# Optimization experiments

Hardware: AMD Instinct MI355X
Metric: run time of the kernel (lower is better)

The kernel has to match this reference:

```python
import jax, jax.numpy as jnp
import numpy as np

N = 2048      # feature_num (nodes/sensors)
T = 5         # timd_num (window length)
D = 64        # embed_dim
TOPK = 21     # topk + 1 (includes self, cos(i,i)=1)
B = 32        # batch
EPS = 1e-5
NEG_SLOPE = 0.2


def setup_inputs() -> dict:
    key = jax.random.key(0)
    ks = jax.random.split(key, 9)
    s = 1.0 / np.sqrt(D)
    return {
        "x": jax.random.normal(ks[0], (B, N, T), jnp.float32),
        "emb": jax.random.normal(ks[1], (N, D), jnp.float32) * s,      # embedding table
        "W": jax.random.normal(ks[2], (D, T), jnp.float32) * (1.0 / np.sqrt(T)),  # GNN lin weight
        "Wb": jax.random.normal(ks[3], (D,), jnp.float32) * 0.01,       # GNN lin bias
        "a_src": jax.random.normal(ks[4], (2 * D,), jnp.float32) * s,   # attention vec (source half)
        "a_dst": jax.random.normal(ks[5], (2 * D,), jnp.float32) * s,   # attention vec (dest half)
        "gamma": jnp.ones((D,), jnp.float32),                            # BatchNorm1d weight
        "beta": jnp.zeros((D,), jnp.float32),                            # BatchNorm1d bias
        "fc_w": jax.random.normal(ks[6], (1, D), jnp.float32) * s,      # fc weight
        "fc_b": jnp.zeros((1,), jnp.float32),                            # fc bias
    }


def reference(x, emb, W, Wb, a_src, a_dst, gamma, beta, fc_w, fc_b):
    # --- cosine-sim topk graph build ---
    norm = jnp.linalg.norm(emb, axis=-1)                    # [N]
    cos = (emb @ emb.T) / (norm[:, None] * norm[None, :])   # [N,N]
    _, idx = jax.lax.top_k(cos, TOPK)                       # [N,TOPK]
    # scatter one-hot adjacency (vectorized, no per-row loop)
    adj = jnp.zeros((N, N), x.dtype).at[jnp.arange(N)[:, None], idx].set(1.0)
    # --- GNN: GDN-style attention message passing ---
    h = jnp.einsum('bnt,dt->bnd', x, W) + Wb                # [B,N,D]
    g = jnp.concatenate([h, jnp.broadcast_to(emb, h.shape)], axis=-1)  # [B,N,2D]
    e_src = g @ a_src                                       # [B,N]
    e_dst = g @ a_dst                                       # [B,N]
    e = jax.nn.leaky_relu(e_src[:, :, None] + e_dst[:, None, :], NEG_SLOPE)  # [B,N,N]
    e = jnp.where(adj > 0, e, jnp.float32(-1e9))
    alpha = jax.nn.softmax(e, axis=-1)                      # [B,N,N], rows sum to 1 over TOPK nbrs
    z = jax.nn.relu(jnp.einsum('bij,bjd->bid', alpha, h))   # [B,N,D]
    # --- output head: z * emb, BN over channels, relu, fc ---
    out = z * emb                                           # [B,N,D]
    mean = out.mean(axis=(0, 1))                            # BN1d stats over (batch, nodes)
    var = out.var(axis=(0, 1))
    out = (out - mean) * jax.lax.rsqrt(var + EPS) * gamma + beta
    out = jax.nn.relu(out)
    out = out @ fc_w.T + fc_b                               # [B,N,1]
    return out.reshape(-1, N)                               # [B,N]
```

## Files before the change

### kernel.cpp

```cpp
#include <hip/hip_runtime.h>
#include <hip/hip_fp16.h>
#include <math.h>

#define N_NODES 2048
#define T_WIN 5
#define D_EMB 64
#define TOPK 21
#define B_BATCH 32
#define BN_TOTAL (B_BATCH * N_NODES)
#define EPS_BN 1e-5f
#define NEG_SLOPE 0.2f
#define STATS_STRIDE 16

typedef unsigned long long u64;
typedef unsigned short u16;
typedef unsigned int u32;

__device__ __forceinline__ float wave_sum(float v) {
#pragma unroll
    for (int off = 32; off > 0; off >>= 1) v += __shfl_xor(v, off, 64);
    return v;
}

__device__ __forceinline__ u64 max64(u64 a, u64 b) { return a > b ? a : b; }
__device__ __forceinline__ u64 min64(u64 a, u64 b) { return a < b ? a : b; }

__device__ __forceinline__ u64 bitonic_sort64_desc(u64 key, int lane) {
#pragma unroll
    for (int k = 2; k <= 64; k <<= 1) {
#pragma unroll
        for (int j = k >> 1; j >= 1; j >>= 1) {
            u64 pk = __shfl_xor(key, j, 64);
            bool dirDesc = ((lane & k) == 0);
            bool keepMax = (((lane & j) == 0) == dirDesc);
            key = keepMax ? max64(key, pk) : min64(key, pk);
        }
    }
    return key;
}

__device__ __forceinline__ u64 bitonic_merge_top64(u64 a, u64 b, int lane) {
    u64 br = __shfl(b, 63 - lane, 64);
    u64 c = max64(a, br);
#pragma unroll
    for (int j = 32; j >= 1; j >>= 1) {
        u64 pk = __shfl_xor(c, j, 64);
        bool keepMax = ((lane & j) == 0);
        c = keepMax ? max64(c, pk) : min64(c, pk);
    }
    return c;
}

__device__ __forceinline__ u16 f2bf(float f) {
    unsigned u = __float_as_uint(f);
    return (u16)((u + 0x7FFFu + ((u >> 16) & 1u)) >> 16);
}
__device__ __forceinline__ float bf2f(u16 h) {
    return __uint_as_float((unsigned)h << 16);
}

__global__ __launch_bounds__(256) void k_preg(
    const float* __restrict__ x, const float* __restrict__ W,
    const float* __restrict__ Wb, const float* __restrict__ a_src,
    const float* __restrict__ a_dst, const float* __restrict__ emb,
    float* __restrict__ xs2T, float* __restrict__ xd2T,
    float* __restrict__ es_embP, float* __restrict__ ed_embP,
    float* __restrict__ norms, float* __restrict__ dotM,
    float* __restrict__ stats, float* __restrict__ stats2) {
    __shared__ __align__(16) float As[64][68];
    __shared__ __align__(16) float Bs[64][68];
    int t = threadIdx.x;

    if (blockIdx.x >= 528) {
        int eb = blockIdx.x - 528;
        if (eb < 512) {
            if (eb < 2) {
                float* p = eb ? stats2 : stats;
                ((float4*)p)[t] = make_float4(0.f, 0.f, 0.f, 0.f);
            }
            int wid = t >> 6, lane = t & 63;
            int node = eb * 4 + wid;
            float e = emb[node * D_EMB + lane];
            float s2 = wave_sum(e * e);
            float esE = wave_sum(e * a_src[D_EMB + lane]);
            float edE = wave_sum(e * a_dst[D_EMB + lane]);
            if (lane == 0) {
                norms[node] = sqrtf(s2);
                es_embP[node] = esE;
                ed_embP[node] = edE;
            }
        } else {
            __shared__ float cws[5], cwd[5], cbs[2];
            if (t < 12) {
                int which = (t < 5 || t == 10) ? 0 : 1;
                const float* av = which ? a_dst : a_src;
                const float* sp;
                int stride;
                if (t < 10) { int tt = (t < 5) ? t : t - 5; sp = W + tt; stride = T_WIN; }
                else        { sp = Wb; stride = 1; }
                float acc = 0.f;
                for (int d = 0; d < D_EMB; d++) acc += sp[d * stride] * av[d];
                if (t < 5)       cws[t] = acc;
                else if (t < 10) cwd[t - 5] = acc;
                else             cbs[t - 10] = acc;
            }
            __syncthreads();
            float ws0 = cws[0], ws1 = cws[1], ws2 = cws[2], ws3 = cws[3], ws4 = cws[4];
            float wd0 = cwd[0], wd1 = cwd[1], wd2 = cwd[2], wd3 = cwd[3], wd4 = cwd[4];
            float bss = cbs[0], bsd = cbs[1];
            int base = (eb - 512) * 1024;
#pragma unroll
            for (int r = 0; r < 4; r++) {
                int item = base + 256 * r + t;
                const float* xp = x + (size_t)item * T_WIN;
                float x0 = xp[0], x1 = xp[1], x2 = xp[2], x3 = xp[3], x4 = xp[4];
                xs2T[item] = bss + x0 * ws0 + x1 * ws1 + x2 * ws2 + x3 * ws3 + x4 * ws4;
                xd2T[item] = bsd + x0 * wd0 + x1 * wd1 + x2 * wd2 + x3 * wd3 + x4 * wd4;
            }
        }
        return;
    }

    int g = blockIdx.x;
    int a = (int)((sqrtf(8.f * g + 1.f) - 1.f) * 0.5f);
    while ((a + 1) * (a + 2) / 2 <= g) a++;
    while (a * (a + 1) / 2 > g) a--;
    int bq = g - a * (a + 1) / 2;
    int i0 = a * 64, j0 = bq * 64;

    {
        int r = t >> 2, c0 = t & 3;
        const float4* srcA = (const float4*)(emb + (size_t)(i0 + r) * D_EMB);
        const float4* srcB = (const float4*)(emb + (size_t)(j0 + r) * D_EMB);
#pragma unroll
        for (int k = 0; k < 4; k++) {
            int f4 = c0 + 4 * k;
            float4 v = srcA[f4];
            int d = 4 * f4;
            As[d][r] = v.x; As[d + 1][r] = v.y; As[d + 2][r] = v.z; As[d + 3][r] = v.w;
            float4 w = srcB[f4];
            Bs[d][r] = w.x; Bs[d + 1][r] = w.y; Bs[d + 2][r] = w.z; Bs[d + 3][r] = w.w;
        }
    }
    __syncthreads();

    int ti = t & 15, tj = t >> 4;
    float acc[4][4] = {};
#pragma unroll
    for (int d = 0; d < 64; d++) {
        float4 av = *(const float4*)&As[d][4 * ti];
        float4 bv = *(const float4*)&Bs[d][4 * tj];
        acc[0][0] += av.x * bv.x; acc[0][1] += av.x * bv.y; acc[0][2] += av.x * bv.z; acc[0][3] += av.x * bv.w;
        acc[1][0] += av.y * bv.x; acc[1][1] += av.y * bv.y; acc[1][2] += av.y * bv.z; acc[1][3] += av.y * bv.w;
        acc[2][0] += av.z * bv.x; acc[2][1] += av.z * bv.y; acc[2][2] += av.z * bv.z; acc[2][3] += av.z * bv.w;
        acc[3][0] += av.w * bv.x; acc[3][1] += av.w * bv.y; acc[3][2] += av.w * bv.z; acc[3][3] += av.w * bv.w;
    }

#pragma unroll
    for (int r = 0; r < 4; r++) {
        float4 o;
        o.x = acc[r][0]; o.y = acc[r][1]; o.z = acc[r][2]; o.w = acc[r][3];
        int i = i0 + 4 * ti + r;
        *(float4*)(dotM + (size_t)i * N_NODES + j0 + 4 * tj) = o;
        dotM[(size_t)(j0 + 4 * tj + 0) * N_NODES + i] = o.x;
        dotM[(size_t)(j0 + 4 * tj + 1) * N_NODES + i] = o.y;
        dotM[(size_t)(j0 + 4 * tj + 2) * N_NODES + i] = o.z;
        dotM[(size_t)(j0 + 4 * tj + 3) * N_NODES + i] = o.w;
    }
}

__global__ __launch_bounds__(256) void k_select(
    const float* __restrict__ dotM, const float* __restrict__ norms,
    int* __restrict__ idxT) {
    __shared__ u64 candbuf[4][128];
    __shared__ u64 mbuf[2][64];
    int tid = threadIdx.x;
    int wid = tid >> 6, lane = tid & 63;
    int pair = wid >> 1;
    int half = wid & 1;
    int i = blockIdx.x * 2 + pair;
    int jbase = half * (N_NODES / 2);
    const float* row = dotM + (size_t)i * N_NODES + jbase;
    u64* buf = candbuf[wid];
    float ni = norms[i];

    u64 a = 0;
    u64 t = 0;
    int cnt = 0;
    float vcur = row[lane];
    float ncur = norms[jbase + lane];

#pragma unroll 1
    for (int c = 0; c < N_NODES / 128; c++) {
        int j = c * 64 + lane;
        float dv = vcur, nv = ncur;
        if (c < N_NODES / 128 - 1) {
            vcur = row[j + 64];
            ncur = norms[jbase + j + 64];
        }
        float v = dv / (ni * nv);
        unsigned u = __float_as_uint(v);
        u = (u & 0x80000000u) ? ~u : (u | 0x80000000u);
        u64 key = ((u64)u << 32) | (unsigned)(~(j + jbase));
        unsigned long long ball = __ballot(key > t);
        if (ball) {
            int ofs = __popcll(ball & ((1ull << lane) - 1ull));
            if (key > t) buf[cnt + ofs] = key;
            cnt += (int)__popcll(ball);
            if (cnt >= 64) {
                u64 nk = buf[lane];
                nk = bitonic_sort64_desc(nk, lane);
                a = bitonic_merge_top64(a, nk, lane);
                t = __shfl(a, 20, 64);
                int rem = cnt - 64;
                u64 mv = (lane < rem) ? buf[64 + lane] : 0;
                if (lane < rem) buf[lane] = mv;
                cnt = rem;
            }
        }
    }
    while (cnt > 0) {
        int take = cnt < 64 ? cnt : 64;
        u64 nk = (lane < take) ? buf[lane] : 0;
        nk = bitonic_sort64_desc(nk, lane);
        a = bitonic_merge_top64(a, nk, lane);
        t = __shfl(a, 20, 64);
        int rem = cnt - take;
        u64 mv = (lane < rem) ? buf[take + lane] : 0;
        if (lane < rem) buf[lane] = mv;
        cnt = rem;
    }

    if (half) mbuf[pair][lane] = a;
    __syncthreads();
    if (!half) {
        u64 bv = mbuf[pair][lane];
        a = bitonic_merge_top64(a, bv, lane);
        if (lane < TOPK) idxT[lane * N_NODES + i] = (int)(~(unsigned)a);
    }
}

__global__ __launch_bounds__(256) void k_alpha(
    const int* __restrict__ idxT, const float* __restrict__ xs2T,
    const float* __restrict__ xd2T, const float* __restrict__ es_embP,
    const float* __restrict__ ed_embP, u32* __restrict__ paT) {
    __shared__ float sed[N_NODES];
    int g = blockIdx.x;
    int b = g & 31;
    int i0 = (g >> 5) * 256;
    int t = threadIdx.x;

    {
        const float4* sxd = (const float4*)(xd2T + (size_t)b * N_NODES);
        const float4* sde = (const float4*)(ed_embP);
        float4* dst = (float4*)sed;
#pragma unroll
        for (int q = 0; q < 2; q++) {
            int idx = t + 256 * q;
            float4 u = sxd[idx];
            float4 v = sde[idx];
            dst[idx] = make_float4(u.x + v.x, u.y + v.y, u.z + v.z, u.w + v.w);
        }
    }
    __syncthreads();

    int i = i0 + t;
    float es = xs2T[(size_t)b * N_NODES + i] + es_embP[i];
    int jk[TOPK];
    float ev[TOPK];
    float m = -3e38f;
#pragma unroll
    for (int k = 0; k < TOPK; k++) {
        jk[k] = idxT[k * N_NODES + i];
        float e = es + sed[jk[k]];
        e = e > 0.f ? e : NEG_SLOPE * e;
        ev[k] = e;
        m = fmaxf(m, e);
    }
    float s = 0.f;
#pragma unroll
    for (int k = 0; k < TOPK; k++) {
        ev[k] = __expf(ev[k] - m);
        s += ev[k];
    }
    float inv = 1.0f / s;
#pragma unroll
    for (int k = 0; k < TOPK; k++) {
        u16 ah = __half_as_ushort(__float2half_rn(ev[k] * inv));
        paT[((size_t)b * TOPK + k) * N_NODES + i] = ((u32)jk[k] << 16) | (u32)ah;
    }
}

__global__ __launch_bounds__(256, 4) void k_msg(
    const float* __restrict__ x, const float* __restrict__ W,
    const float* __restrict__ Wb, const u32* __restrict__ paT,
    const float* __restrict__ emb, uint4* __restrict__ obufT,
    float* __restrict__ stats, float* __restrict__ stats2) {
    __shared__ __align__(16) u32 hts[N_NODES][4];
    __shared__ float sred[2][4][8];

    int g = blockIdx.x;
    int b = g & 31;
    int cc = (g >> 5) & 7;
    int half = g >> 8;
    int d0 = cc * 8;
    int ibase = half * (N_NODES / 2);
    int t = threadIdx.x;
    int wid = t >> 6, lane = t & 63;

    float wc[8][T_WIN], wb8[8];
#pragma unroll
    for (int q = 0; q < 8; q++) {
        wb8[q] = Wb[d0 + q];
#pragma unroll
        for (int tt = 0; tt < T_WIN; tt++) wc[q][tt] = W[(d0 + q) * T_WIN + tt];
    }
    const float* xb = x + (size_t)b * N_NODES * T_WIN;
#pragma unroll
    for (int r = 0; r < 8; r++) {
        int row = t + 256 * r;
        const float* xr = xb + row * T_WIN;
        float x0 = xr[0], x1 = xr[1], x2 = xr[2], x3 = xr[3], x4 = xr[4];
        float h[8];
#pragma unroll
        for (int q = 0; q < 8; q++)
            h[q] = wb8[q] + x0 * wc[q][0] + x1 * wc[q][1] + x2 * wc[q][2]
                 + x3 * wc[q][3] + x4 * wc[q][4];
        __half2 p0 = __floats2half2_rn(h[0], h[1]);
        __half2 p1 = __floats2half2_rn(h[2], h[3]);
        __half2 p2 = __floats2half2_rn(h[4], h[5]);
        __half2 p3 = __floats2half2_rn(h[6], h[7]);
        uint4 sv;
        sv.x = *(u32*)&p0; sv.y = *(u32*)&p1; sv.z = *(u32*)&p2; sv.w = *(u32*)&p3;
        *(uint4*)&hts[row][0] = sv;
    }
    __syncthreads();

    float sacc[8] = {}, sacc2[8] = {};
    const u32* pb = paT + (size_t)b * TOPK * N_NODES;
#pragma unroll 1
    for (int r = 0; r < 4; r++) {
        int i = ibase + 256 * r + t;
        __half2 z01 = __floats2half2_rn(0.f, 0.f);
        __half2 z23 = z01, z45 = z01, z67 = z01;
#pragma unroll
        for (int k = 0; k < TOPK; k++) {
            u32 pa = pb[(size_t)k * N_NODES + i];
            int jk = (int)(pa >> 16);
            __half2 av = __half2half2(__ushort_as_half((u16)(pa & 0xFFFFu)));
            uint4 hv = *(const uint4*)&hts[jk][0];
            z01 = __hfma2(av, *(__half2*)&hv.x, z01);
            z23 = __hfma2(av, *(__half2*)&hv.y, z23);
            z45 = __hfma2(av, *(__half2*)&hv.z, z45);
            z67 = __hfma2(av, *(__half2*)&hv.w, z67);
        }
        float2 f01 = __half22float2(z01);
        float2 f23 = __half22float2(z23);
        float2 f45 = __half22float2(z45);
        float2 f67 = __half22float2(z67);
        float4 e0 = *(const float4*)(emb + (size_t)i * D_EMB + d0);
        float4 e1 = *(const float4*)(emb + (size_t)i * D_EMB + d0 + 4);
        float o[8];
        o[0] = fmaxf(f01.x, 0.f) * e0.x;
        o[1] = fmaxf(f01.y, 0.f) * e0.y;
        o[2] = fmaxf(f23.x, 0.f) * e0.z;
        o[3] = fmaxf(f23.y, 0.f) * e0.w;
        o[4] = fmaxf(f45.x, 0.f) * e1.x;
        o[5] = fmaxf(f45.y, 0.f) * e1.y;
        o[6] = fmaxf(f67.x, 0.f) * e1.z;
        o[7] = fmaxf(f67.y, 0.f) * e1.w;
        uint4 st;
        st.x = (u32)f2bf(o[0]) | ((u32)f2bf(o[1]) << 16);
        st.y = (u32)f2bf(o[2]) | ((u32)f2bf(o[3]) << 16);
        st.z = (u32)f2bf(o[4]) | ((u32)f2bf(o[5]) << 16);
        st.w = (u32)f2bf(o[6]) | ((u32)f2bf(o[7]) << 16);
        obufT[((size_t)cc * B_BATCH + b) * N_NODES + i] = st;
#pragma unroll
        for (int q = 0; q < 8; q++) {
            sacc[q] += o[q];
            sacc2[q] += o[q] * o[q];
        }
    }

#pragma unroll
    for (int q = 0; q < 8; q++) {
        sacc[q] = wave_sum(sacc[q]);
        sacc2[q] = wave_sum(sacc2[q]);
    }
    if (lane == 0) {
#pragma unroll
        for (int q = 0; q < 8; q++) {
            sred[0][wid][q] = sacc[q];
            sred[1][wid][q] = sacc2[q];
        }
    }
    __syncthreads();
    if (t < 16) {
        int q = t & 7, which = t >> 3;
        float v = sred[which][0][q] + sred[which][1][q] + sred[which][2][q] + sred[which][3][q];
        float* dst = which ? stats2 : stats;
        atomicAdd(&dst[(d0 + q) * STATS_STRIDE], v);
    }
}

__global__ __launch_bounds__(256) void k_out(
    const uint4* __restrict__ obufT, const float* __restrict__ stats,
    const float* __restrict__ stats2, const float* __restrict__ gamma,
    const float* __restrict__ beta, const float* __restrict__ fc_w,
    const float* __restrict__ fc_b, float* __restrict__ out) {
    __shared__ float smean[64], sinv[64], sg[64], sb[64], sf[64];
    int t = threadIdx.x;
    int g = blockIdx.x;
    int b = g & 31, nc = g >> 5;
    int n = nc * 256 + t;
    const float invM = 1.0f / (float)BN_TOTAL;

    if (t < 64) {
        float mn = stats[t * STATS_STRIDE] * invM;
        float var = stats2[t * STATS_STRIDE] * invM - mn * mn;
        smean[t] = mn;
        sinv[t] = rsqrtf(var + EPS_BN);
        sg[t] = gamma[t]; sb[t] = beta[t]; sf[t] = fc_w[t];
    }
    __syncthreads();

    float fb = fc_b[0];
    float p = 0.f;
#pragma unroll
    for (int cc = 0; cc < 8; cc++) {
        uint4 hv = obufT[((size_t)cc * B_BATCH + b) * N_NODES + n];
        int d = cc * 8;
        float o[8];
        o[0] = bf2f((u16)(hv.x & 0xFFFFu)); o[1] = bf2f((u16)(hv.x >> 16));
        o[2] = bf2f((u16)(hv.y & 0xFFFFu)); o[3] = bf2f((u16)(hv.y >> 16));
        o[4] = bf2f((u16)(hv.z & 0xFFFFu)); o[5] = bf2f((u16)(hv.z >> 16));
        o[6] = bf2f((u16)(hv.w & 0xFFFFu)); o[7] = bf2f((u16)(hv.w >> 16));
#pragma unroll
        for (int q = 0; q < 8; q++) {
            float v = fmaxf((o[q] - smean[d + q]) * sinv[d + q] * sg[d + q] + sb[d + q], 0.f);
            p = fmaf(v, sf[d + q], p);
        }
    }
    out[b * N_NODES + n] = p + fb;
}

extern "C" void kernel_launch(void* const* d_in, const int* in_sizes, int n_in,
                              void* d_out, int out_size, void* d_ws, size_t ws_size,
                              hipStream_t stream) {
    const float* x     = (const float*)d_in[0];
    const float* emb   = (const float*)d_in[1];
    const float* W     = (const float*)d_in[2];
    const float* Wb    = (const float*)d_in[3];
    const float* a_src = (const float*)d_in[4];
    const float* a_dst = (const float*)d_in[5];
    const float* gamma = (const float*)d_in[6];
    const float* beta  = (const float*)d_in[7];
    const float* fc_w  = (const float*)d_in[8];
    const float* fc_b  = (const float*)d_in[9];
    float* out = (float*)d_out;

    char* ws = (char*)d_ws;
    float* stats   = (float*)(ws + 0);
    float* stats2  = (float*)(ws + 4096);
    int*   idxT    = (int*)  (ws + 8192);
    float* norms   = (float*)(ws + 180224);
    float* es_embP = (float*)(ws + 188416);
    float* ed_embP = (float*)(ws + 196608);
    float* xs2T    = (float*)(ws + 204800);
    float* xd2T    = (float*)(ws + 466944);
    u32*   paT     = (u32*)  (ws + 729088);
    float* dotM    = (float*)(ws + 6234112);
    uint4* obufT   = (uint4*)dotM;

    k_preg<<<1104, 256, 0, stream>>>(x, W, Wb, a_src, a_dst, emb,
                                     xs2T, xd2T, es_embP, ed_embP, norms,
                                     dotM, stats, stats2);
    k_select<<<N_NODES / 2, 256, 0, stream>>>(dotM, norms, idxT);
    k_alpha<<<256, 256, 0, stream>>>(idxT, xs2T, xd2T, es_embP, ed_embP, paT);
    k_msg<<<512, 256, 0, stream>>>(x, W, Wb, paT, emb, obufT, stats, stats2);
    k_out<<<256, 256, 0, stream>>>(obufT, stats, stats2, gamma, beta, fc_w, fc_b, out);
}
```

Measured before the change: 126.2 us.

## Fuse top-k selection with attention softmax and store per-node packed neighbor segments

Merges the top-k select kernel and the alpha/softmax kernel into one, so each select block computes softmax weights for its two rows across all 32 batches straight from shared-memory neighbor indices. This drops a launch and the idxT round trip. The packed alpha/index array changes from a k-major transposed layout to contiguous 24-word segments per (node, batch). The message kernel can then load all 21 entries with vector loads instead of 21 strided loads. The trade-off is gathered, uncoalesced reads of xd2T inside the select kernel and a strided row access pattern in k_msg.

```diff
diff --git a/kernel.cpp b/kernel.cpp
--- a/kernel.cpp
+++ b/kernel.cpp
@@ -11,6 +11,7 @@
 #define EPS_BN 1e-5f
 #define NEG_SLOPE 0.2f
 #define STATS_STRIDE 16
+#define PA_STRIDE 24
 
 typedef unsigned long long u64;
 typedef unsigned short u16;
@@ -169,11 +170,14 @@
     }
 }
 
-__global__ __launch_bounds__(256) void k_select(
+__global__ __launch_bounds__(256) void k_selal(
     const float* __restrict__ dotM, const float* __restrict__ norms,
-    int* __restrict__ idxT) {
+    const float* __restrict__ xs2T, const float* __restrict__ xd2T,
+    const float* __restrict__ es_embP, const float* __restrict__ ed_embP,
+    u32* __restrict__ paT) {
     __shared__ u64 candbuf[4][128];
     __shared__ u64 mbuf[2][64];
+    __shared__ int sjk[2][PA_STRIDE];
     int tid = threadIdx.x;
     int wid = tid >> 6, lane = tid & 63;
     int pair = wid >> 1;
@@ -236,58 +240,53 @@
     if (!half) {
         u64 bv = mbuf[pair][lane];
         a = bitonic_merge_top64(a, bv, lane);
-        if (lane < TOPK) idxT[lane * N_NODES + i] = (int)(~(unsigned)a);
-    }
-}
-
-__global__ __launch_bounds__(256) void k_alpha(
-    const int* __restrict__ idxT, const float* __restrict__ xs2T,
-    const float* __restrict__ xd2T, const float* __restrict__ es_embP,
-    const float* __restrict__ ed_embP, u32* __restrict__ paT) {
-    __shared__ float sed[N_NODES];
-    int g = blockIdx.x;
-    int b = g & 31;
-    int i0 = (g >> 5) * 256;
-    int t = threadIdx.x;
+        if (lane < TOPK) sjk[pair][lane] = (int)(~(unsigned)a);
+    }
+    __syncthreads();
 
     {
-        const float4* sxd = (const float4*)(xd2T + (size_t)b * N_NODES);
-        const float4* sde = (const float4*)(ed_embP);
-        float4* dst = (float4*)sed;
-#pragma unroll
-        for (int q = 0; q < 2; q++) {
-            int idx = t + 256 * q;
-            float4 u = sxd[idx];
-            float4 v = sde[idx];
-            dst[idx] = make_float4(u.x + v.x, u.y + v.y, u.z + v.z, u.w + v.w);
-        }
-    }
-    __syncthreads();
-
-    int i = i0 + t;
-    float es = xs2T[(size_t)b * N_NODES + i] + es_embP[i];
-    int jk[TOPK];
-    float ev[TOPK];
-    float m = -3e38f;
-#pragma unroll
-    for (int k = 0; k < TOPK; k++) {
-        jk[k] = idxT[k * N_NODES + i];
-        float e = es + sed[jk[k]];
-        e = e > 0.f ? e : NEG_SLOPE * e;
-        ev[k] = e;
-        m = fmaxf(m, e);
-    }
-    float s = 0.f;
-#pragma unroll
-    for (int k = 0; k < TOPK; k++) {
-        ev[k] = __expf(ev[k] - m);
-        s += ev[k];
-    }
-    float inv = 1.0f / s;
-#pragma unroll
-    for (int k = 0; k < TOPK; k++) {
-        u16 ah = __half_as_ushort(__float2half_rn(ev[k] * inv));
-        paT[((size_t)b * TOPK + k) * N_NODES + i] = ((u32)jk[k] << 16) | (u32)ah;
+        int p = wid * 16 + (lane >> 2);
+        int prow = p >> 5;
+        int bb = p & 31;
+        int sub = lane & 3;
+        int irow = blockIdx.x * 2 + prow;
+        float es = xs2T[(size_t)bb * N_NODES + irow] + es_embP[irow];
+        float ev[6];
+        int jv[6];
+        float m = -3e38f;
+#pragma unroll
+        for (int q = 0; q < 6; q++) {
+            int k = sub + 4 * q;
+            bool ok = k < TOPK;
+            int kk = ok ? k : 0;
+            int jkv = sjk[prow][kk];
+            float e = es + (xd2T[(size_t)bb * N_NODES + jkv] + ed_embP[jkv]);
+            e = e > 0.f ? e : NEG_SLOPE * e;
+            e = ok ? e : -3e38f;
+            ev[q] = e;
+            jv[q] = jkv;
+            m = fmaxf(m, e);
+        }
+        m = fmaxf(m, __shfl_xor(m, 1, 64));
+        m = fmaxf(m, __shfl_xor(m, 2, 64));
+        float s = 0.f;
+#pragma unroll
+        for (int q = 0; q < 6; q++) {
+            ev[q] = __expf(ev[q] - m);
+            s += ev[q];
+        }
+        s += __shfl_xor(s, 1, 64);
+        s += __shfl_xor(s, 2, 64);
+        float inv = 1.0f / s;
+        u32* seg = paT + ((size_t)irow * B_BATCH + bb) * PA_STRIDE;
+#pragma unroll
+        for (int q = 0; q < 6; q++) {
+            int k = sub + 4 * q;
+            if (k < TOPK) {
+                u16 ah = __half_as_ushort(__float2half_rn(ev[q] * inv));
+                seg[k] = ((u32)jv[q] << 16) | (u32)ah;
+            }
+        }
     }
 }
 
@@ -337,15 +336,26 @@
     __syncthreads();
 
     float sacc[8] = {}, sacc2[8] = {};
-    const u32* pb = paT + (size_t)b * TOPK * N_NODES;
 #pragma unroll 1
     for (int r = 0; r < 4; r++) {
         int i = ibase + 256 * r + t;
+        const u32* seg = paT + ((size_t)i * B_BATCH + b) * PA_STRIDE;
+        const uint4* seg4 = (const uint4*)seg;
+        uint4 va = seg4[0], vb = seg4[1], vc4 = seg4[2], vd = seg4[3], ve = seg4[4];
+        u32 p20 = seg[20];
+        u32 pk[21];
+        pk[0] = va.x;  pk[1] = va.y;  pk[2] = va.z;  pk[3] = va.w;
+        pk[4] = vb.x;  pk[5] = vb.y;  pk[6] = vb.z;  pk[7] = vb.w;
+        pk[8] = vc4.x; pk[9] = vc4.y; pk[10] = vc4.z; pk[11] = vc4.w;
+        pk[12] = vd.x; pk[13] = vd.y; pk[14] = vd.z; pk[15] = vd.w;
+        pk[16] = ve.x; pk[17] = ve.y; pk[18] = ve.z; pk[19] = ve.w;
+        pk[20] = p20;
+
         __half2 z01 = __floats2half2_rn(0.f, 0.f);
         __half2 z23 = z01, z45 = z01, z67 = z01;
 #pragma unroll
         for (int k = 0; k < TOPK; k++) {
-            u32 pa = pb[(size_t)k * N_NODES + i];
+            u32 pa = pk[k];
             int jk = (int)(pa >> 16);
             __half2 av = __half2half2(__ushort_as_half((u16)(pa & 0xFFFFu)));
             uint4 hv = *(const uint4*)&hts[jk][0];
@@ -462,21 +472,20 @@
     char* ws = (char*)d_ws;
     float* stats   = (float*)(ws + 0);
     float* stats2  = (float*)(ws + 4096);
-    int*   idxT    = (int*)  (ws + 8192);
-    float* norms   = (float*)(ws + 180224);
-    float* es_embP = (float*)(ws + 188416);
-    float* ed_embP = (float*)(ws + 196608);
-    float* xs2T    = (float*)(ws + 204800);
-    float* xd2T    = (float*)(ws + 466944);
-    u32*   paT     = (u32*)  (ws + 729088);
-    float* dotM    = (float*)(ws + 6234112);
+    float* norms   = (float*)(ws + 8192);
+    float* es_embP = (float*)(ws + 16384);
+    float* ed_embP = (float*)(ws + 24576);
+    float* xs2T    = (float*)(ws + 32768);
+    float* xd2T    = (float*)(ws + 294912);
+    u32*   paT     = (u32*)  (ws + 557056);
+    float* dotM    = (float*)(ws + 6848512);
     uint4* obufT   = (uint4*)dotM;
 
     k_preg<<<1104, 256, 0, stream>>>(x, W, Wb, a_src, a_dst, emb,
                                      xs2T, xd2T, es_embP, ed_embP, norms,
                                      dotM, stats, stats2);
-    k_select<<<N_NODES / 2, 256, 0, stream>>>(dotM, norms, idxT);
-    k_alpha<<<256, 256, 0, stream>>>(idxT, xs2T, xd2T, es_embP, ed_embP, paT);
+    k_selal<<<N_NODES / 2, 256, 0, stream>>>(dotM, norms, xs2T, xd2T,
+                                             es_embP, ed_embP, paT);
     k_msg<<<512, 256, 0, stream>>>(x, W, Wb, paT, emb, obufT, stats, stats2);
     k_out<<<256, 256, 0, stream>>>(obufT, stats, stats2, gamma, beta, fc_w, fc_b, out);
 }
```

After: 128.3 us. About the same (+1.6%).
